# Kernel optimization log

Hardware: AMD Instinct MI355X
Metric: run time of the kernel (lower is better)

The kernel has to match this reference:

```python
import jax, jax.numpy as jnp
import numpy as np
from jax import lax

DIM = 192
HEADS = 8
HIDDEN = int(DIM * 2.66)  # 510
EPS_LN = 1e-5
EPS_NORM = 1e-12


def conv1x1(x, w):
    # x: (B,C,H,W), w: (O,I,1,1)
    return lax.conv_general_dilated(x, w, (1, 1), 'VALID',
                                    dimension_numbers=('NCHW', 'OIHW', 'NCHW'))


def dwconv3x3(x, w):
    # depthwise 3x3, padding=1; w: (C,1,3,3)
    c = x.shape[1]
    return lax.conv_general_dilated(x, w, (1, 1), 'SAME',
                                    dimension_numbers=('NCHW', 'OIHW', 'NCHW'),
                                    feature_group_count=c)


def layernorm_chan(x, weight, bias):
    # WithBias LayerNorm over channel dim of NCHW (matches to_3d -> LN(-1) -> to_4d)
    mu = jnp.mean(x, axis=1, keepdims=True)
    var = jnp.var(x, axis=1, keepdims=True)
    xn = (x - mu) * lax.rsqrt(var + EPS_LN)
    return xn * weight[None, :, None, None] + bias[None, :, None, None]


def l2norm(x):
    # F.normalize along last dim with eps=1e-12
    n = jnp.sqrt(jnp.sum(x * x, axis=-1, keepdims=True))
    return x / jnp.maximum(n, EPS_NORM)


def attention(x, temperature, w_qkv, w_qkv_dw, w_proj):
    b, c, h, w = x.shape
    hw = h * w
    head_dim = c // HEADS
    qkv = dwconv3x3(conv1x1(x, w_qkv), w_qkv_dw)  # (B, 3C, H, W)
    q, k, v = jnp.split(qkv, 3, axis=1)
    q = l2norm(q.reshape(b, HEADS, head_dim, hw))
    k = l2norm(k.reshape(b, HEADS, head_dim, hw))
    v = v.reshape(b, HEADS, head_dim, hw)
    # channel-wise attention: (B,H,d,d)
    attn = jnp.einsum('bhde,bhce->bhdc', q, k) * temperature[None]
    attn = jax.nn.softmax(attn, axis=-1)
    out = jnp.einsum('bhdc,bhce->bhde', attn, v).reshape(b, c, h, w)
    return conv1x1(out, w_proj)


def ffn(x, w_in, w_dw, w_out):
    x = conv1x1(x, w_in)                 # (B, 2*hidden, H, W)
    x = dwconv3x3(x, w_dw)
    x1, x2 = jnp.split(x, 2, axis=1)
    x = jax.nn.gelu(x1, approximate=False) * x2
    return conv1x1(x, w_out)


def setup_inputs() -> dict:
    key = jax.random.key(0)
    ks = jax.random.split(key, 8)
    b, c, h, w = 4, DIM, 128, 128
    s = 0.05
    return {
        'x': jax.random.normal(ks[0], (b, c, h, w), jnp.float32),
        'temperature': jnp.ones((HEADS, 1, 1), jnp.float32),
        'ln1_w': jnp.ones((c,), jnp.float32),
        'ln1_b': jnp.zeros((c,), jnp.float32),
        'ln2_w': jnp.ones((c,), jnp.float32),
        'ln2_b': jnp.zeros((c,), jnp.float32),
        'w_qkv': jax.random.normal(ks[1], (3 * c, c, 1, 1), jnp.float32) * s,
        'w_qkv_dw': jax.random.normal(ks[2], (3 * c, 1, 3, 3), jnp.float32) * s,
        'w_proj': jax.random.normal(ks[3], (c, c, 1, 1), jnp.float32) * s,
        'w_in': jax.random.normal(ks[4], (2 * HIDDEN, c, 1, 1), jnp.float32) * s,
        'w_dw': jax.random.normal(ks[5], (2 * HIDDEN, 1, 3, 3), jnp.float32) * s,
        'w_out_ffn': jax.random.normal(ks[6], (c, HIDDEN, 1, 1), jnp.float32) * s,
    }


def reference(x, temperature, ln1_w, ln1_b, ln2_w, ln2_b, w_qkv, w_qkv_dw,
              w_proj, w_in, w_dw, w_out_ffn):
    x = x + attention(layernorm_chan(x, ln1_w, ln1_b), temperature,
                      w_qkv, w_qkv_dw, w_proj)
    x = x + ffn(layernorm_chan(x, ln2_w, ln2_b), w_in, w_dw, w_out_ffn)
    return x
```

## Files before the change

### kernel.cpp

```cpp
#include <hip/hip_runtime.h>
#include <hip/hip_bf16.h>
#include <math.h>


#define HW_ 16384

typedef __attribute__((ext_vector_type(8))) short bf16x8;
typedef __attribute__((ext_vector_type(4))) float f32x4;
typedef __attribute__((ext_vector_type(16))) float f32x16;
typedef __attribute__((ext_vector_type(4))) int i32x4;

union Pack8 { __hip_bfloat16 h[8]; i32x4 v; };

__global__ __launch_bounds__(256) void convert_weights(
    const float* __restrict__ wqkv, const float* __restrict__ wproj,
    const float* __restrict__ win, const float* __restrict__ wout,
    __hip_bfloat16* __restrict__ oq, __hip_bfloat16* __restrict__ op,
    __hip_bfloat16* __restrict__ oi, __hip_bfloat16* __restrict__ oo) {
  const int i = blockIdx.x * 256 + threadIdx.x;
  if (i < 110592) oq[i] = __float2bfloat16(wqkv[i]);
  if (i < 36864)  op[i] = __float2bfloat16(wproj[i]);
  if (i < 196608) {
    int m = i / 192, k = i - m * 192;
    oi[i] = __float2bfloat16(m < 1020 ? win[m * 192 + k] : 0.f);
  }
  if (i < 98304) {
    int m = i >> 9, k = i & 511;
    oo[i] = __float2bfloat16(k < 510 ? wout[m * 510 + k] : 0.f);
  }
}

__global__ __launch_bounds__(256) void ln_t_kernel(
    const float* __restrict__ x, const float* __restrict__ w,
    const float* __restrict__ bi, __hip_bfloat16* __restrict__ yt) {
  const int b = blockIdx.y;
  x += (size_t)b * 192 * HW_;
  yt += (size_t)b * HW_ * 192;
  __shared__ float tile[192][68];
  __shared__ float psum[4][64], psq[4][64];
  __shared__ float mu_s[64], inv_s[64];
  const int tid = threadIdx.x;
  const int p0 = blockIdx.x * 64;
  for (int idx = tid; idx < 192 * 16; idx += 256) {
    int c = idx >> 4, p4 = idx & 15;
    f32x4 v = *(const f32x4*)(x + (size_t)c * HW_ + p0 + p4 * 4);
    *(f32x4*)&tile[c][p4 * 4] = v;
  }
  __syncthreads();
  const int tx = tid & 63, ty = tid >> 6;
  float s = 0.f, s2 = 0.f;
  for (int c = ty * 48; c < ty * 48 + 48; c++) {
    float v = tile[c][tx]; s += v; s2 += v * v;
  }
  psum[ty][tx] = s; psq[ty][tx] = s2;
  __syncthreads();
  if (ty == 0) {
    float ts = psum[0][tx] + psum[1][tx] + psum[2][tx] + psum[3][tx];
    float ts2 = psq[0][tx] + psq[1][tx] + psq[2][tx] + psq[3][tx];
    float mu = ts * (1.f / 192.f);
    float var = ts2 * (1.f / 192.f) - mu * mu;
    mu_s[tx] = mu; inv_s[tx] = rsqrtf(var + 1e-5f);
  }
  __syncthreads();
  for (int idx = tid; idx < 64 * 24; idx += 256) {
    int c8 = idx % 24, p = idx / 24;
    float mu = mu_s[p], inv = inv_s[p];
    Pack8 pk;
    #pragma unroll
    for (int u = 0; u < 8; u++) {
      int c = c8 * 8 + u;
      pk.h[u] = __float2bfloat16((tile[c][p] - mu) * inv * w[c] + bi[c]);
    }
    *(i32x4*)&yt[(size_t)(p0 + p) * 192 + c8 * 8] = pk.v;
  }
}

template <int EPI>
__global__ __launch_bounds__(256) void gemm_bstat(
    const __hip_bfloat16* __restrict__ A, const __hip_bfloat16* __restrict__ Bg,
    const float* __restrict__ Cres, void* __restrict__ Dout,
    int Mtiles, size_t Bstr, size_t Cstr, size_t Dstr) {
  const int z = blockIdx.y;
  const __hip_bfloat16* B = Bg + (size_t)z * Bstr;
  const int col0 = blockIdx.x * 128;
  __shared__ __align__(16) __hip_bfloat16 Bs[128][192];
  const int tid = threadIdx.x;
  const int wave = tid >> 6, lane = tid & 63;
  const int quad = lane >> 4, lr = lane & 15;
  const int wm = (wave & 1) * 32, wn = (wave >> 1) * 64;
  const int lrx = lr & 7;

  const int arow = tid >> 3, ach = tid & 7;
  const int achs = ach ^ (arow & 7);
  #pragma unroll
  for (int l = 0; l < 4; l++) {
    const int row = arow + 32 * l;
    const __hip_bfloat16* bp = B + (size_t)(col0 + row) * 192;
    #pragma unroll
    for (int j = 0; j < 3; j++) {
      i32x4 v = *(const i32x4*)(bp + (ach + 8 * j) * 8);
      *(i32x4*)&Bs[row][(achs + 8 * j) * 8] = v;
    }
  }
  __syncthreads();

  const __hip_bfloat16* Ar0 = A + (size_t)(wm + lr) * 192 + quad * 8;
  const __hip_bfloat16* Ar1 = A + (size_t)(wm + 16 + lr) * 192 + quad * 8;

  for (int mt = 0; mt < Mtiles; mt++) {
    const size_t abase = (size_t)mt * (64 * 192);
    bf16x8 a0[6], a1[6];
    #pragma unroll
    for (int kc = 0; kc < 6; kc++) {
      a0[kc] = *(const bf16x8*)(Ar0 + abase + kc * 32);
      a1[kc] = *(const bf16x8*)(Ar1 + abase + kc * 32);
    }
    f32x4 acc[2][4];
    #pragma unroll
    for (int i = 0; i < 2; i++)
      #pragma unroll
      for (int j = 0; j < 4; j++) acc[i][j] = (f32x4){0.f, 0.f, 0.f, 0.f};
    #pragma unroll
    for (int kc = 0; kc < 6; kc++) {
      const int chq = ((kc * 4 + quad) ^ lrx) * 8;
      #pragma unroll
      for (int j = 0; j < 4; j++) {
        bf16x8 bb = *(const bf16x8*)&Bs[wn + j * 16 + lr][chq];
        acc[0][j] = __builtin_amdgcn_mfma_f32_16x16x32_bf16(a0[kc], bb, acc[0][j], 0, 0, 0);
        acc[1][j] = __builtin_amdgcn_mfma_f32_16x16x32_bf16(a1[kc], bb, acc[1][j], 0, 0, 0);
      }
    }
    const int row0 = mt * 64;
    #pragma unroll
    for (int i = 0; i < 2; i++) {
      #pragma unroll
      for (int r = 0; r < 4; r++) {
        const int gm = row0 + wm + i * 16 + quad * 4 + r;
        const size_t base = (size_t)gm * HW_ + col0 + wn + lr;
        if (EPI == 0) {
          __hip_bfloat16* dp = (__hip_bfloat16*)Dout + (size_t)z * Dstr + base;
          #pragma unroll
          for (int j = 0; j < 4; j++) dp[j * 16] = __float2bfloat16(acc[i][j][r]);
        } else {
          float* dp = (float*)Dout + (size_t)z * Dstr + base;
          const float* cp = Cres + (size_t)z * Cstr + base;
          #pragma unroll
          for (int j = 0; j < 4; j++) dp[j * 16] = acc[i][j][r] + cp[j * 16];
        }
      }
    }
  }
}

template <int EPI>
__global__ __launch_bounds__(256) void mfma_gemm(
    const __hip_bfloat16* __restrict__ A, const __hip_bfloat16* __restrict__ Bg,
    const float* __restrict__ Cres, void* __restrict__ Dout,
    int M, int N, int K, size_t Bstr, size_t Cstr, size_t Dstr) {
  const int z = blockIdx.z;
  const __hip_bfloat16* B = Bg + (size_t)z * Bstr;
  const float* C = Cres ? Cres + (size_t)z * Cstr : nullptr;
  __shared__ __align__(16) __hip_bfloat16 As[64][64];
  __shared__ __align__(16) __hip_bfloat16 Bs[128][64];
  const int tid = threadIdx.x;
  const int wave = tid >> 6, lane = tid & 63;
  const int quad = lane >> 4, lr = lane & 15;
  const int lrx = lr & 7;
  const int wm = (wave & 1) * 32, wn = (wave >> 1) * 64;
  const int row0 = blockIdx.x * 64, col0 = blockIdx.y * 128;

  f32x4 acc[2][4];
  #pragma unroll
  for (int i = 0; i < 2; i++)
    #pragma unroll
    for (int j = 0; j < 4; j++) acc[i][j] = (f32x4){0.f, 0.f, 0.f, 0.f};

  for (int k0 = 0; k0 < K; k0 += 64) {
    #pragma unroll
    for (int l = 0; l < 2; l++) {
      int t = tid + l * 256;
      int row = t >> 3, ch = t & 7;
      i32x4 v = *(const i32x4*)(A + (size_t)(row0 + row) * K + k0 + ch * 8);
      *(i32x4*)&As[row][(ch ^ (row & 7)) * 8] = v;
    }
    #pragma unroll
    for (int l = 0; l < 4; l++) {
      int t = tid + l * 256;
      int row = t >> 3, ch = t & 7;
      i32x4 v = *(const i32x4*)(B + (size_t)(col0 + row) * K + k0 + ch * 8);
      *(i32x4*)&Bs[row][(ch ^ (row & 7)) * 8] = v;
    }
    __syncthreads();
    #pragma unroll
    for (int ks = 0; ks < 2; ks++) {
      const int chq = ((ks * 4 + quad) ^ lrx) * 8;
      bf16x8 a0 = *(const bf16x8*)&As[wm + lr][chq];
      bf16x8 a1 = *(const bf16x8*)&As[wm + 16 + lr][chq];
      #pragma unroll
      for (int j = 0; j < 4; j++) {
        bf16x8 bb = *(const bf16x8*)&Bs[wn + j * 16 + lr][chq];
        acc[0][j] = __builtin_amdgcn_mfma_f32_16x16x32_bf16(a0, bb, acc[0][j], 0, 0, 0);
        acc[1][j] = __builtin_amdgcn_mfma_f32_16x16x32_bf16(a1, bb, acc[1][j], 0, 0, 0);
      }
    }
    __syncthreads();
  }

  #pragma unroll
  for (int i = 0; i < 2; i++) {
    #pragma unroll
    for (int r = 0; r < 4; r++) {
      int gm = row0 + wm + i * 16 + quad * 4 + r;
      if (gm >= M) continue;
      #pragma unroll
      for (int j = 0; j < 4; j++) {
        int gn = col0 + wn + j * 16 + lr;
        size_t idx = (size_t)gm * N + gn;
        if (EPI == 0) {
          (((__hip_bfloat16*)Dout) + (size_t)z * Dstr)[idx] = __float2bfloat16(acc[i][j][r]);
        } else {
          (((float*)Dout) + (size_t)z * Dstr)[idx] = acc[i][j][r] + C[idx];
        }
      }
    }
  }
}

__global__ __launch_bounds__(256) void dw_kernel(
    const __hip_bfloat16* __restrict__ in, const float* __restrict__ wdw,
    __hip_bfloat16* __restrict__ out, float* __restrict__ nrm2p) {
  const int b = blockIdx.z;
  in  += (size_t)b * 576 * HW_;
  out += (size_t)b * 576 * HW_;
  const int c = blockIdx.y;
  const int x8 = threadIdx.x & 15;
  const int y = blockIdx.x * 16 + (threadIdx.x >> 4);
  const __hip_bfloat16* ip = in + (size_t)c * HW_;
  const float* wp = wdw + c * 9;
  float wv[9];
  #pragma unroll
  for (int u = 0; u < 9; u++) wv[u] = wp[u];
  float acc[8];
  #pragma unroll
  for (int j = 0; j < 8; j++) acc[j] = 0.f;
  #pragma unroll
  for (int r = 0; r < 3; r++) {
    const int yy = y + r - 1;
    const bool valid = (yy >= 0) && (yy < 128);
    Pack8 mid;
    if (valid) mid.v = *(const i32x4*)(ip + yy * 128 + x8 * 8);
    else       mid.v = (i32x4){0, 0, 0, 0};
    const int hi = ((i32x4)mid.v)[3];
    const int lo = ((i32x4)mid.v)[0];
    const int lw = __shfl_up(hi, 1, 64);
    const int rw = __shfl_down(lo, 1, 64);
    float row[10];
    row[0] = (x8 > 0) ? (float)(((const __hip_bfloat16*)&lw)[1]) : 0.f;
    #pragma unroll
    for (int u = 0; u < 8; u++) row[1 + u] = (float)mid.h[u];
    row[9] = (x8 < 15) ? (float)(((const __hip_bfloat16*)&rw)[0]) : 0.f;
    const float wl = wv[r * 3], wc = wv[r * 3 + 1], wr = wv[r * 3 + 2];
    #pragma unroll
    for (int j = 0; j < 8; j++)
      acc[j] += wl * row[j] + wc * row[j + 1] + wr * row[j + 2];
  }
  Pack8 o;
  #pragma unroll
  for (int j = 0; j < 8; j++) o.h[j] = __float2bfloat16(acc[j]);
  *(i32x4*)(out + (size_t)c * HW_ + y * 128 + x8 * 8) = o.v;
  if (c < 384) {
    float s = 0.f;
    #pragma unroll
    for (int j = 0; j < 8; j++) s += acc[j] * acc[j];
    #pragma unroll
    for (int off = 32; off > 0; off >>= 1) s += __shfl_down(s, off, 64);
    __shared__ float wsum[4];
    const int lane = threadIdx.x & 63, wvi = threadIdx.x >> 6;
    if (lane == 0) wsum[wvi] = s;
    __syncthreads();
    if (threadIdx.x == 0)
      nrm2p[((size_t)b * 384 + c) * 8 + blockIdx.x] =
          wsum[0] + wsum[1] + wsum[2] + wsum[3];
  }
}

__global__ __launch_bounds__(256) void gram_kernel(
    const __hip_bfloat16* __restrict__ qkv, float* __restrict__ Gpart) {
  const int b = blockIdx.z;
  qkv   += (size_t)b * 576 * HW_;
  Gpart += (size_t)b * 32 * 8 * 576;
  const int h = blockIdx.x, chunk = blockIdx.y;
  const int tid = threadIdx.x;
  const int w = tid >> 6, lane = tid & 63;
  const int m = lane & 31;
  const int khalf = lane >> 5;
  const __hip_bfloat16* qb = qkv + (size_t)(h * 24) * HW_;
  const __hip_bfloat16* kb = qkv + (size_t)(192 + h * 24) * HW_;
  f32x16 acc;
  #pragma unroll
  for (int i = 0; i < 16; i++) acc[i] = 0.f;
  const int e0 = chunk * 512 + w * 128;
  #pragma unroll
  for (int j = 0; j < 8; j++) {
    const int k0 = e0 + j * 16 + khalf * 8;
    bf16x8 a = *(const bf16x8*)(qb + (size_t)m * HW_ + k0);
    bf16x8 bfr = *(const bf16x8*)(kb + (size_t)m * HW_ + k0);
    acc = __builtin_amdgcn_mfma_f32_32x32x16_bf16(a, bfr, acc, 0, 0, 0);
  }
  __shared__ float gs[4][576];
  #pragma unroll
  for (int r = 0; r < 16; r++) {
    int row = (r & 3) + 8 * (r >> 2) + 4 * khalf;
    if (row < 24 && m < 24) gs[w][row * 24 + m] = acc[r];
  }
  __syncthreads();
  float* gp = Gpart + (size_t)(chunk * 8 + h) * 576;
  for (int t = tid; t < 576; t += 256)
    gp[t] = gs[0][t] + gs[1][t] + gs[2][t] + gs[3][t];
}

__global__ __launch_bounds__(256) void softmax2_kernel(
    const float* __restrict__ Gpart, const float* __restrict__ nrm2p,
    const float* __restrict__ temp, float* __restrict__ P) {
  const int b = blockIdx.y;
  Gpart += (size_t)b * 32 * 8 * 576;
  nrm2p += (size_t)b * 384 * 8;
  P     += (size_t)b * 8 * 576;
  const int h = blockIdx.x;
  const int tid = threadIdx.x;
  __shared__ float Gs[576];
  __shared__ float nq[24], nk[24];
  for (int t = tid; t < 576; t += 256) {
    float s = 0.f;
    for (int ch = 0; ch < 32; ch++)
      s += Gpart[(size_t)(ch * 8 + h) * 576 + t];
    Gs[t] = s;
  }
  if (tid < 48) {
    const int r = (tid < 24) ? (h * 24 + tid) : (192 + h * 24 + tid - 24);
    float s = 0.f;
    #pragma unroll
    for (int j = 0; j < 8; j++) s += nrm2p[(size_t)r * 8 + j];
    float nv = fmaxf(sqrtf(s), 1e-12f);
    if (tid < 24) nq[tid] = nv; else nk[tid - 24] = nv;
  }
  __syncthreads();
  if (tid < 24) {
    const int d = tid;
    const float tp = temp[h];
    float row[24], mx = -1e30f;
    #pragma unroll
    for (int c = 0; c < 24; c++) {
      float v = Gs[d * 24 + c] * tp / (nq[d] * nk[c]);
      row[c] = v; mx = fmaxf(mx, v);
    }
    float s = 0.f;
    #pragma unroll
    for (int c = 0; c < 24; c++) { float e = expf(row[c] - mx); row[c] = e; s += e; }
    const float inv = 1.f / s;
    #pragma unroll
    for (int c = 0; c < 24; c++) P[h * 576 + d * 24 + c] = row[c] * inv;
  }
}

__global__ __launch_bounds__(256) void pv_kernel(
    const float* __restrict__ P, const __hip_bfloat16* __restrict__ qkv,
    __hip_bfloat16* __restrict__ yt) {
  const int b = blockIdx.z;
  P   += (size_t)b * 8 * 576;
  qkv += (size_t)b * 576 * HW_;
  yt  += (size_t)b * HW_ * 192;
  const int hh = blockIdx.x;
  const int e = blockIdx.y * 256 + threadIdx.x;
  __shared__ float Ps[576];
  for (int t = threadIdx.x; t < 576; t += 256) Ps[t] = P[hh * 576 + t];
  __syncthreads();
  const __hip_bfloat16* vb = qkv + (size_t)(384 + hh * 24) * HW_;
  float acc[24];
  #pragma unroll
  for (int d = 0; d < 24; d++) acc[d] = 0.f;
  for (int c = 0; c < 24; c++) {
    float v = (float)vb[(size_t)c * HW_ + e];
    #pragma unroll
    for (int d = 0; d < 24; d++) acc[d] += Ps[d * 24 + c] * v;
  }
  #pragma unroll
  for (int g = 0; g < 3; g++) {
    Pack8 pk;
    #pragma unroll
    for (int u = 0; u < 8; u++) pk.h[u] = __float2bfloat16(acc[g * 8 + u]);
    *(i32x4*)&yt[(size_t)e * 192 + hh * 24 + g * 8] = pk.v;
  }
}

__global__ __launch_bounds__(256) void dwg_t_kernel(
    const __hip_bfloat16* __restrict__ hsrc, const float* __restrict__ wdw,
    __hip_bfloat16* __restrict__ gt, int b0) {
  const int z = blockIdx.z;
  const int bb = b0 + z;
  const int yt = blockIdx.x >> 1, xh = blockIdx.x & 1;
  const int cz = blockIdx.y;
  const int tid = threadIdx.x;
  const int cl = tid >> 3, x8 = tid & 7;
  const int c = cz * 32 + cl;
  const int y0 = yt * 8;
  const int pxb = xh * 64 + x8 * 8;
  __shared__ __hip_bfloat16 sg[32][522];

  const bool active = (c < 510);
  const int ca = active ? c : 0;
  const __hip_bfloat16* ha = hsrc + ((size_t)bb * 1024 + ca) * HW_;
  const __hip_bfloat16* hb = hsrc + ((size_t)bb * 1024 + ca + 510) * HW_;
  float wva[9], wvb[9];
  #pragma unroll
  for (int u = 0; u < 9; u++) {
    wva[u] = active ? wdw[c * 9 + u] : 0.f;
    wvb[u] = active ? wdw[(c + 510) * 9 + u] : 0.f;
  }

  float aA[3][8], aB[3][8];
  #pragma unroll
  for (int s = 0; s < 3; s++)
    #pragma unroll
    for (int j = 0; j < 8; j++) { aA[s][j] = 0.f; aB[s][j] = 0.f; }

  #pragma unroll
  for (int i = 0; i < 10; i++) {
    const int ry = y0 - 1 + i;
    float ra[10], rb[10];
    if (ry >= 0 && ry < 128) {
      const int off = ry * 128 + pxb;
      Pack8 ma; ma.v = *(const i32x4*)(ha + off);
      Pack8 mb; mb.v = *(const i32x4*)(hb + off);
      ra[0] = (pxb > 0) ? (float)ha[off - 1] : 0.f;
      rb[0] = (pxb > 0) ? (float)hb[off - 1] : 0.f;
      #pragma unroll
      for (int u = 0; u < 8; u++) { ra[1 + u] = (float)ma.h[u]; rb[1 + u] = (float)mb.h[u]; }
      ra[9] = (pxb < 120) ? (float)ha[off + 8] : 0.f;
      rb[9] = (pxb < 120) ? (float)hb[off + 8] : 0.f;
    } else {
      #pragma unroll
      for (int u = 0; u < 10; u++) { ra[u] = 0.f; rb[u] = 0.f; }
    }
    #pragma unroll
    for (int r = 0; r < 3; r++) {
      const int lo = i - r;
      if (lo < 0 || lo >= 8) continue;
      const int s = lo % 3;
      const float a0 = wva[r * 3], a1 = wva[r * 3 + 1], a2 = wva[r * 3 + 2];
      const float b0w = wvb[r * 3], b1 = wvb[r * 3 + 1], b2 = wvb[r * 3 + 2];
      #pragma unroll
      for (int j = 0; j < 8; j++) {
        aA[s][j] += a0 * ra[j] + a1 * ra[j + 1] + a2 * ra[j + 2];
        aB[s][j] += b0w * rb[j] + b1 * rb[j + 1] + b2 * rb[j + 2];
      }
    }
    {
      const int lo = i - 2;
      if (lo >= 0 && lo < 8) {
        const int s = lo % 3;
        Pack8 o;
        #pragma unroll
        for (int j = 0; j < 8; j++) {
          float v = aA[s][j];
          float ge = 0.5f * v * (1.f + erff(v * 0.70710678118654752f));
          o.h[j] = __float2bfloat16(ge * aB[s][j]);
          aA[s][j] = 0.f; aB[s][j] = 0.f;
        }
        *(i32x4*)&sg[cl][lo * 64 + x8 * 8] = o.v;
      }
    }
  }
  __syncthreads();
  const int sp = tid >> 2, ch0 = (tid & 3) * 8;
  #pragma unroll
  for (int k = 0; k < 8; k++) {
    Pack8 o;
    #pragma unroll
    for (int u = 0; u < 8; u++) o.h[u] = sg[ch0 + u][k * 64 + sp];
    const int gp = (y0 + k) * 128 + xh * 64 + sp;
    *(i32x4*)&gt[((size_t)z * HW_ + gp) * 512 + cz * 32 + ch0] = o.v;
  }
}

extern "C" void kernel_launch(void* const* d_in, const int* in_sizes, int n_in,
                              void* d_out, int out_size, void* d_ws, size_t ws_size,
                              hipStream_t stream) {
  const float* x     = (const float*)d_in[0];
  const float* temp  = (const float*)d_in[1];
  const float* ln1w  = (const float*)d_in[2];
  const float* ln1b  = (const float*)d_in[3];
  const float* ln2w  = (const float*)d_in[4];
  const float* ln2b  = (const float*)d_in[5];
  const float* wqkv  = (const float*)d_in[6];
  const float* wqkvdw= (const float*)d_in[7];
  const float* wproj = (const float*)d_in[8];
  const float* win   = (const float*)d_in[9];
  const float* wdw   = (const float*)d_in[10];
  const float* wout  = (const float*)d_in[11];
  float* out = (float*)d_out;
  char* ws = (char*)d_ws;

  const int HW = 16384;
  const size_t HWC = (size_t)192 * HW;

  __hip_bfloat16* yt    = (__hip_bfloat16*)(ws + 0);
  __hip_bfloat16* qkva  = (__hip_bfloat16*)(ws + 25165824);
  __hip_bfloat16* qkvb  = (__hip_bfloat16*)(ws + 100663296);
  __hip_bfloat16* hbuf  = (__hip_bfloat16*)(ws + 25165824);
  float*          xa    = (float*)(ws + 176160768);
  __hip_bfloat16* gt    = (__hip_bfloat16*)(ws + 226492416);
  __hip_bfloat16* wqkvB = (__hip_bfloat16*)(ws + 260046848);
  __hip_bfloat16* wprojB= (__hip_bfloat16*)(ws + 260268032);
  __hip_bfloat16* winB  = (__hip_bfloat16*)(ws + 260341760);
  __hip_bfloat16* woutB = (__hip_bfloat16*)(ws + 260734976);
  float*          nrm2p = (float*)(ws + 260931584);
  float*          Gpart = (float*)(ws + 260980736);
  float*          P     = (float*)(ws + 263340032);

  convert_weights<<<768, 256, 0, stream>>>(wqkv, wproj, win, wout,
                                           wqkvB, wprojB, winB, woutB);

  ln_t_kernel<<<dim3(256, 4), 256, 0, stream>>>(x, ln1w, ln1b, yt);
  gemm_bstat<0><<<dim3(128, 4), 256, 0, stream>>>(
      wqkvB, yt, nullptr, qkva, 9, (size_t)HW * 192, 0, (size_t)576 * HW);
  dw_kernel<<<dim3(8, 576, 4), 256, 0, stream>>>(qkva, wqkvdw, qkvb, nrm2p);
  gram_kernel<<<dim3(8, 32, 4), 256, 0, stream>>>(qkvb, Gpart);
  softmax2_kernel<<<dim3(8, 4), 256, 0, stream>>>(Gpart, nrm2p, temp, P);
  pv_kernel<<<dim3(8, 64, 4), 256, 0, stream>>>(P, qkvb, yt);
  gemm_bstat<1><<<dim3(128, 4), 256, 0, stream>>>(
      wprojB, yt, x, xa, 3, (size_t)HW * 192, HWC, HWC);
  ln_t_kernel<<<dim3(256, 4), 256, 0, stream>>>(xa, ln2w, ln2b, yt);
  gemm_bstat<0><<<dim3(128, 4), 256, 0, stream>>>(
      winB, yt, nullptr, hbuf, 16, (size_t)HW * 192, 0, (size_t)1024 * HW);
  for (int half = 0; half < 2; half++) {
    const int b0 = half * 2;
    dwg_t_kernel<<<dim3(32, 16, 2), 256, 0, stream>>>(hbuf, wdw, gt, b0);
    mfma_gemm<1><<<dim3(3, 128, 2), 256, 0, stream>>>(
        woutB, gt, xa + (size_t)b0 * HWC, out + (size_t)b0 * HWC,
        192, HW, 512, (size_t)HW * 512, HWC, HWC);
  }
}
```

Before: 517.0 us.

## Stage weight tiles through LDS with register prefetch; halve dwconv row tile

gemm_bstat now loads each 64x192 weight tile cooperatively into swizzled shared memory and prefetches the next tile into registers while the current tile's MFMAs run. Previously every wave read its A fragments straight from global memory. This adds two barriers per M tile. Separately, the FFN depthwise+GELU kernel processes 4 rows per block instead of 8, doubling the grid and shrinking LDS use to raise parallelism, at the cost of more halo-row reloads.

```diff
diff --git a/kernel.cpp b/kernel.cpp
--- a/kernel.cpp
+++ b/kernel.cpp
@@ -84,6 +84,7 @@
   const __hip_bfloat16* B = Bg + (size_t)z * Bstr;
   const int col0 = blockIdx.x * 128;
   __shared__ __align__(16) __hip_bfloat16 Bs[128][192];
+  __shared__ __align__(16) __hip_bfloat16 As[64][192];
   const int tid = threadIdx.x;
   const int wave = tid >> 6, lane = tid & 63;
   const int quad = lane >> 4, lr = lane & 15;
@@ -92,6 +93,7 @@
 
   const int arow = tid >> 3, ach = tid & 7;
   const int achs = ach ^ (arow & 7);
+
   #pragma unroll
   for (int l = 0; l < 4; l++) {
     const int row = arow + 32 * l;
@@ -102,18 +104,30 @@
       *(i32x4*)&Bs[row][(achs + 8 * j) * 8] = v;
     }
   }
-  __syncthreads();
-
-  const __hip_bfloat16* Ar0 = A + (size_t)(wm + lr) * 192 + quad * 8;
-  const __hip_bfloat16* Ar1 = A + (size_t)(wm + 16 + lr) * 192 + quad * 8;
+  i32x4 areg[6];
+  #pragma unroll
+  for (int l = 0; l < 2; l++)
+    #pragma unroll
+    for (int j = 0; j < 3; j++)
+      areg[l * 3 + j] = *(const i32x4*)(
+          A + (size_t)(arow + 32 * l) * 192 + (ach + 8 * j) * 8);
+  #pragma unroll
+  for (int l = 0; l < 2; l++)
+    #pragma unroll
+    for (int j = 0; j < 3; j++)
+      *(i32x4*)&As[arow + 32 * l][(achs + 8 * j) * 8] = areg[l * 3 + j];
+  __syncthreads();
 
   for (int mt = 0; mt < Mtiles; mt++) {
-    const size_t abase = (size_t)mt * (64 * 192);
-    bf16x8 a0[6], a1[6];
-    #pragma unroll
-    for (int kc = 0; kc < 6; kc++) {
-      a0[kc] = *(const bf16x8*)(Ar0 + abase + kc * 32);
-      a1[kc] = *(const bf16x8*)(Ar1 + abase + kc * 32);
+    const int row0 = mt * 64;
+    if (mt + 1 < Mtiles) {
+      const __hip_bfloat16* ap = A + (size_t)(mt + 1) * 64 * 192;
+      #pragma unroll
+      for (int l = 0; l < 2; l++)
+        #pragma unroll
+        for (int j = 0; j < 3; j++)
+          areg[l * 3 + j] = *(const i32x4*)(
+              ap + (size_t)(arow + 32 * l) * 192 + (ach + 8 * j) * 8);
     }
     f32x4 acc[2][4];
     #pragma unroll
@@ -123,16 +137,17 @@
     #pragma unroll
     for (int kc = 0; kc < 6; kc++) {
       const int chq = ((kc * 4 + quad) ^ lrx) * 8;
+      bf16x8 a0 = *(const bf16x8*)&As[wm + lr][chq];
+      bf16x8 a1 = *(const bf16x8*)&As[wm + 16 + lr][chq];
       #pragma unroll
       for (int j = 0; j < 4; j++) {
         bf16x8 bb = *(const bf16x8*)&Bs[wn + j * 16 + lr][chq];
-        acc[0][j] = __builtin_amdgcn_mfma_f32_16x16x32_bf16(a0[kc], bb, acc[0][j], 0, 0, 0);
-        acc[1][j] = __builtin_amdgcn_mfma_f32_16x16x32_bf16(a1[kc], bb, acc[1][j], 0, 0, 0);
+        acc[0][j] = __builtin_amdgcn_mfma_f32_16x16x32_bf16(a0, bb, acc[0][j], 0, 0, 0);
+        acc[1][j] = __builtin_amdgcn_mfma_f32_16x16x32_bf16(a1, bb, acc[1][j], 0, 0, 0);
       }
     }
-    const int row0 = mt * 64;
-    #pragma unroll
-    for (int i = 0; i < 2; i++) {
+    #pragma unroll
+    for (int i = 0; i < 2; i++)
       #pragma unroll
       for (int r = 0; r < 4; r++) {
         const int gm = row0 + wm + i * 16 + quad * 4 + r;
@@ -148,6 +163,14 @@
           for (int j = 0; j < 4; j++) dp[j * 16] = acc[i][j][r] + cp[j * 16];
         }
       }
+    __syncthreads();
+    if (mt + 1 < Mtiles) {
+      #pragma unroll
+      for (int l = 0; l < 2; l++)
+        #pragma unroll
+        for (int j = 0; j < 3; j++)
+          *(i32x4*)&As[arow + 32 * l][(achs + 8 * j) * 8] = areg[l * 3 + j];
+      __syncthreads();
     }
   }
 }
@@ -403,9 +426,9 @@
   const int tid = threadIdx.x;
   const int cl = tid >> 3, x8 = tid & 7;
   const int c = cz * 32 + cl;
-  const int y0 = yt * 8;
+  const int y0 = yt * 4;
   const int pxb = xh * 64 + x8 * 8;
-  __shared__ __hip_bfloat16 sg[32][522];
+  __shared__ __hip_bfloat16 sg[32][266];
 
   const bool active = (c < 510);
   const int ca = active ? c : 0;
@@ -425,7 +448,7 @@
     for (int j = 0; j < 8; j++) { aA[s][j] = 0.f; aB[s][j] = 0.f; }
 
   #pragma unroll
-  for (int i = 0; i < 10; i++) {
+  for (int i = 0; i < 6; i++) {
     const int ry = y0 - 1 + i;
     float ra[10], rb[10];
     if (ry >= 0 && ry < 128) {
@@ -445,7 +468,7 @@
     #pragma unroll
     for (int r = 0; r < 3; r++) {
       const int lo = i - r;
-      if (lo < 0 || lo >= 8) continue;
+      if (lo < 0 || lo >= 4) continue;
       const int s = lo % 3;
       const float a0 = wva[r * 3], a1 = wva[r * 3 + 1], a2 = wva[r * 3 + 2];
       const float b0w = wvb[r * 3], b1 = wvb[r * 3 + 1], b2 = wvb[r * 3 + 2];
@@ -457,7 +480,7 @@
     }
     {
       const int lo = i - 2;
-      if (lo >= 0 && lo < 8) {
+      if (lo >= 0 && lo < 4) {
         const int s = lo % 3;
         Pack8 o;
         #pragma unroll
@@ -474,7 +497,7 @@
   __syncthreads();
   const int sp = tid >> 2, ch0 = (tid & 3) * 8;
   #pragma unroll
-  for (int k = 0; k < 8; k++) {
+  for (int k = 0; k < 4; k++) {
     Pack8 o;
     #pragma unroll
     for (int u = 0; u < 8; u++) o.h[u] = sg[ch0 + u][k * 64 + sp];
@@ -535,7 +558,7 @@
       winB, yt, nullptr, hbuf, 16, (size_t)HW * 192, 0, (size_t)1024 * HW);
   for (int half = 0; half < 2; half++) {
     const int b0 = half * 2;
-    dwg_t_kernel<<<dim3(32, 16, 2), 256, 0, stream>>>(hbuf, wdw, gt, b0);
+    dwg_t_kernel<<<dim3(64, 16, 2), 256, 0, stream>>>(hbuf, wdw, gt, b0);
     mfma_gemm<1><<<dim3(3, 128, 2), 256, 0, stream>>>(
         woutB, gt, xa + (size_t)b0 * HWC, out + (size_t)b0 * HWC,
         192, HW, 512, (size_t)HW * 512, HWC, HWC);
```

New measurement: 464.6 us. 1.11x faster.
